# Optimization experiments

Hardware: AMD Instinct MI355X
Metric: run time of the kernel (lower is better)

## Reference

```python
import jax, jax.numpy as jnp
import numpy as np

EPS = 1e-5  # BatchNorm eps (torch default)


def gcn_conv(x, W, b, src, dst, ew, n_nodes):
    """PyG GCNConv with normalize=True, add_self_loops=True (fill_value=1.0).
    Self-loop contribution handled analytically instead of appending edges."""
    xw = x @ W  # [N, out]
    # degree including self-loop weight 1.0 (PyG sums weights at the target node)
    deg = jax.ops.segment_sum(ew, dst, num_segments=n_nodes) + 1.0  # [N]
    dinv = jnp.where(deg > 0, jax.lax.rsqrt(deg), 0.0)
    norm = dinv[src] * ew * dinv[dst]  # [E]
    agg = jax.ops.segment_sum(xw[src] * norm[:, None], dst, num_segments=n_nodes)
    agg = agg + xw * (dinv * dinv)[:, None]  # self-loop message
    return agg + b


def batch_norm(x, gamma, beta):
    m = jnp.mean(x, axis=0)
    v = jnp.var(x, axis=0)  # biased, matches torch BN normalization
    return gamma * (x - m) * jax.lax.rsqrt(v + EPS) + beta


def setup_inputs() -> dict:
    key = jax.random.key(0)
    ks = jax.random.split(key, 12)
    N, E, D_IN, D_H, D_OUT = 100000, 1600000, 128, 128, 40
    x = jax.random.normal(ks[0], (N, D_IN), dtype=jnp.float32)
    edge_index = jax.random.randint(ks[1], (2, E), 0, N, dtype=jnp.int64)
    edge_weight = jax.random.uniform(ks[2], (E,), dtype=jnp.float32)
    def lin(k, fi, fo):
        s = 1.0 / np.sqrt(fi)
        return jax.random.uniform(k, (fi, fo), dtype=jnp.float32, minval=-s, maxval=s)
    return {
        "x": x, "edge_index": edge_index, "edge_weight": edge_weight,
        "W0": lin(ks[3], D_IN, D_H), "b0": jnp.zeros((D_H,), jnp.float32),
        "g0": jnp.ones((D_H,), jnp.float32), "be0": jnp.zeros((D_H,), jnp.float32),
        "W1": lin(ks[4], D_H, D_H), "b1": jnp.zeros((D_H,), jnp.float32),
        "g1": jnp.ones((D_H,), jnp.float32), "be1": jnp.zeros((D_H,), jnp.float32),
        "W2": lin(ks[5], D_H, D_OUT), "b2": jnp.zeros((D_OUT,), jnp.float32),
    }


def reference(x, edge_index, edge_weight, W0, b0, g0, be0, W1, b1, g1, be1, W2, b2):
    n_nodes = x.shape[0]
    src, dst = edge_index[0], edge_index[1]
    # layer 0: GCNConv -> BN -> ReLU (dropout identity: deterministic/eval)
    h = gcn_conv(x, W0, b0, src, dst, edge_weight, n_nodes)
    h = jax.nn.relu(batch_norm(h, g0, be0))
    # layer 1
    h = gcn_conv(h, W1, b1, src, dst, edge_weight, n_nodes)
    h = jax.nn.relu(batch_norm(h, g1, be1))
    # last conv + log_softmax over classes
    h = gcn_conv(h, W2, b2, src, dst, edge_weight, n_nodes)
    return jax.nn.log_softmax(h, axis=-1)
```

## Files before the change

kernel.cpp:

```cpp
#include <hip/hip_runtime.h>
#include <math.h>


#define CHUNK 8192

__device__ __forceinline__ float2 bf2_unpack(unsigned u) {
    float2 r;
    r.x = __uint_as_float(u << 16);
    r.y = __uint_as_float(u & 0xffff0000u);
    return r;
}
__device__ __forceinline__ unsigned bf2_pack(float a, float b) {
    unsigned ua = __float_as_uint(a);
    unsigned ub = __float_as_uint(b);
    ua = (ua + 0x7fffu + ((ua >> 16) & 1u)) >> 16;
    ub = (ub + 0x7fffu + ((ub >> 16) & 1u)) >> 16;
    return ua | (ub << 16);
}

__global__ void k_detect(const unsigned* __restrict__ raw, int nsample, int* __restrict__ flag) {
    int i = blockIdx.x * blockDim.x + threadIdx.x;
    if (i < nsample) {
        if (raw[2 * i + 1] != 0u) atomicOr(flag, 1);
    }
}

__device__ __forceinline__ int edge_src(const unsigned* raw, int e, int E, int is64) {
    return is64 ? (int)raw[2 * (size_t)e] : (int)raw[e];
}
__device__ __forceinline__ int edge_dst(const unsigned* raw, int e, int E, int is64) {
    return is64 ? (int)raw[2 * ((size_t)E + e)] : (int)raw[(size_t)E + e];
}

__global__ __launch_bounds__(256) void k_bhist(const unsigned* __restrict__ raw,
                                               int* __restrict__ bhist, int* __restrict__ chist,
                                               const int* __restrict__ flag,
                                               int E, int NB, int nchunks) {
    __shared__ int h[512];
    int is64 = (*flag == 0);
    for (int c = blockIdx.x; c < nchunks; c += gridDim.x) {
        for (int t = threadIdx.x; t < 512; t += 256) h[t] = 0;
        __syncthreads();
        int base = c * CHUNK;
        int end = (base + CHUNK < E) ? base + CHUNK : E;
        for (int e = base + threadIdx.x; e < end; e += 256) {
            int d = edge_dst(raw, e, E, is64);
            atomicAdd(&h[d >> 8], 1);
        }
        __syncthreads();
        for (int t = threadIdx.x; t < NB; t += 256) {
            int v = h[t];
            chist[(size_t)c * 512 + t] = v;
            if (v) atomicAdd(&bhist[t], v);
        }
        __syncthreads();
    }
}

__global__ __launch_bounds__(512) void k_bscan(const int* __restrict__ bhist,
                                               int* __restrict__ bstart,
                                               int* __restrict__ bcur, int NB) {
    __shared__ int s[512];
    int tid = threadIdx.x;
    int v = (tid < NB) ? bhist[tid] : 0;
    s[tid] = v;
    __syncthreads();
    for (int off = 1; off < 512; off <<= 1) {
        int t = (tid >= off) ? s[tid - off] : 0;
        __syncthreads();
        if (tid >= off) s[tid] += t;
        __syncthreads();
    }
    int ex = s[tid] - v;
    if (tid <= NB) {
        int val = (tid < NB) ? ex : s[NB > 0 ? NB - 1 : 0];
        bstart[tid] = val;
        if (tid < NB) bcur[tid] = val;
    }
}

__global__ __launch_bounds__(256) void k_part(const unsigned* __restrict__ raw,
                                              const float* __restrict__ ew,
                                              const int* __restrict__ chist,
                                              int* __restrict__ bcur, int2* __restrict__ staging,
                                              const int* __restrict__ flag,
                                              int E, int NB, int nchunks) {
    __shared__ int cur[512];
    int is64 = (*flag == 0);
    for (int c = blockIdx.x; c < nchunks; c += gridDim.x) {
        for (int t = threadIdx.x; t < NB; t += 256) {
            int v = chist[(size_t)c * 512 + t];
            cur[t] = v ? atomicAdd(&bcur[t], v) : 0;
        }
        __syncthreads();
        int base = c * CHUNK;
        int end = (base + CHUNK < E) ? base + CHUNK : E;
        for (int e = base + threadIdx.x; e < end; e += 256) {
            int s = edge_src(raw, e, E, is64);
            int d = edge_dst(raw, e, E, is64);
            float w = ew[e];
            int pos = atomicAdd(&cur[d >> 8], 1);
            staging[pos] = make_int2(s | ((d & 255) << 24), __float_as_int(w));
        }
        __syncthreads();
    }
}

__global__ __launch_bounds__(256) void k_bucket(const int* __restrict__ bstart,
                                                const int2* __restrict__ staging,
                                                int* __restrict__ rowptr, float* __restrict__ dinv,
                                                int2* __restrict__ ep, int N, int NB) {
    __shared__ int cnt[256];
    __shared__ float dw[256];
    __shared__ int sc[256];
    __shared__ int cur[256];

    const int b = blockIdx.x;
    const int t = threadIdx.x;
    const int n0 = b << 8;
    const int nn = (N - n0 < 256) ? (N - n0) : 256;
    const int es = bstart[b], ee = bstart[b + 1];

    cnt[t] = 0;
    dw[t] = 0.f;
    __syncthreads();

    for (int j = es + t; j < ee; j += 256) {
        int2 p = staging[j];
        int dl = ((unsigned)p.x) >> 24;
        atomicAdd(&cnt[dl], 1);
        atomicAdd(&dw[dl], __int_as_float(p.y));
    }
    __syncthreads();

    int v = cnt[t];
    sc[t] = v;
    __syncthreads();
    for (int off = 1; off < 256; off <<= 1) {
        int tv = (t >= off) ? sc[t - off] : 0;
        __syncthreads();
        if (t >= off) sc[t] += tv;
        __syncthreads();
    }
    int exoff = sc[t] - v;
    cur[t] = es + exoff;
    if (t < nn) {
        rowptr[n0 + t] = es + exoff;
        dinv[n0 + t] = rsqrtf(dw[t] + 1.0f);
    }
    if (t == 0) rowptr[(n0 + 256 < N) ? (n0 + 256) : N] = ee;
    __syncthreads();

    for (int j = es + t; j < ee; j += 256) {
        int2 p = staging[j];
        int dl = ((unsigned)p.x) >> 24;
        int pos = atomicAdd(&cur[dl], 1);
        ep[pos] = make_int2(p.x & 0x00ffffff, p.y);
    }
}

template <int DOUT, int KC, bool BN>
__global__ __launch_bounds__(256) void k_gemm(
    const float* __restrict__ X, const float* __restrict__ W,
    const float* __restrict__ scale, const float* __restrict__ shift,
    const float* __restrict__ dscale, unsigned* __restrict__ Y, int N)
{
    constexpr int NCH = 128 / KC;
    constexpr int NDW = DOUT / 2;
    __shared__ __align__(16) float Wl[KC * DOUT];
    __shared__ __align__(16) float Xs[4][8 * 128];
    __shared__ float sc_l[128], sh_l[128];

    const int tid = threadIdx.x;
    const int wave = tid >> 6, lane = tid & 63;
    if (BN) {
        if (tid < 128) { sc_l[tid] = scale[tid]; sh_l[tid] = shift[tid]; }
    }
    __syncthreads();

    const int srow = lane >> 3;
    const int skk = (lane & 7) * 16;

    for (int base = blockIdx.x * 32; base < N; base += gridDim.x * 32) {
        {
            int r = base + wave * 8 + srow;
            float4 v[4];
            if (r < N) {
                const float4* p = (const float4*)(X + (size_t)r * 128 + skk);
                v[0] = p[0]; v[1] = p[1]; v[2] = p[2]; v[3] = p[3];
            } else {
                v[0] = v[1] = v[2] = v[3] = make_float4(0.f, 0.f, 0.f, 0.f);
            }
            if (BN) {
                float* vf = (float*)v;
#pragma unroll
                for (int j = 0; j < 16; j++)
                    vf[j] = fmaxf(vf[j] * sc_l[skk + j] + sh_l[skk + j], 0.f);
            }
            float4* q = (float4*)&Xs[wave][srow * 128 + skk];
            q[0] = v[0]; q[1] = v[1]; q[2] = v[2]; q[3] = v[3];
        }

        float acc0[8], acc1[8];
#pragma unroll
        for (int r = 0; r < 8; r++) { acc0[r] = 0.f; acc1[r] = 0.f; }

        for (int ch = 0; ch < NCH; ++ch) {
            __syncthreads();
            for (int idx = tid; idx < KC * DOUT / 4; idx += 256)
                ((float4*)Wl)[idx] = ((const float4*)(W + (size_t)ch * KC * DOUT))[idx];
            __syncthreads();

            for (int k = 0; k < KC; k += 4) {
                float4 a[8];
#pragma unroll
                for (int r = 0; r < 8; r++)
                    a[r] = *(const float4*)&Xs[wave][r * 128 + ch * KC + k];
#pragma unroll
                for (int kk = 0; kk < 4; kk++) {
                    float2 wv = make_float2(0.f, 0.f);
                    if (lane < NDW)
                        wv = *(const float2*)&Wl[(k + kk) * DOUT + 2 * lane];
#pragma unroll
                    for (int r = 0; r < 8; r++) {
                        float av = ((const float*)&a[r])[kk];
                        acc0[r] += av * wv.x;
                        acc1[r] += av * wv.y;
                    }
                }
            }
        }

#pragma unroll
        for (int r = 0; r < 8; r++) {
            int row = base + wave * 8 + r;
            if (row < N && lane < NDW) {
                float rs = dscale[row];
                Y[(size_t)row * NDW + lane] = bf2_pack(acc0[r] * rs, acc1[r] * rs);
            }
        }
    }
}

__global__ __launch_bounds__(256) void k_agg128(
    const unsigned* __restrict__ xw, const int* __restrict__ rowptr,
    const int2* __restrict__ ep, const float* __restrict__ dinv,
    const float* __restrict__ bias, float* __restrict__ h,
    float* __restrict__ bn_sum, float* __restrict__ bn_sq, int N)
{
    __shared__ float redS[512], redQ[512];
    const int lane = threadIdx.x & 63;
    const int wave = threadIdx.x >> 6;
    const int base = blockIdx.x * 64 + wave * 16;
    const float b0 = bias[2 * lane], b1 = bias[2 * lane + 1];
    float s0 = 0.f, s1 = 0.f, q0 = 0.f, q1 = 0.f;

    const int nmax = (N - base < 16) ? (N - base) : 16;
    for (int n = 0; n < nmax; n++) {
        const int i = base + n;
        const int rs = rowptr[i], re = rowptr[i + 1];
        const float di = dinv[i];
        float2 sv = bf2_unpack(xw[(size_t)i * 64 + lane]);
        float acc0 = sv.x, acc1 = sv.y;
        int j = rs;
        for (; j + 4 <= re; j += 4) {
            int2 e0 = ep[j], e1 = ep[j + 1], e2 = ep[j + 2], e3 = ep[j + 3];
            unsigned v0 = xw[(size_t)e0.x * 64 + lane];
            unsigned v1 = xw[(size_t)e1.x * 64 + lane];
            unsigned v2 = xw[(size_t)e2.x * 64 + lane];
            unsigned v3 = xw[(size_t)e3.x * 64 + lane];
            float c0 = __int_as_float(e0.y), c1 = __int_as_float(e1.y);
            float c2 = __int_as_float(e2.y), c3 = __int_as_float(e3.y);
            float2 f0 = bf2_unpack(v0), f1 = bf2_unpack(v1);
            float2 f2 = bf2_unpack(v2), f3 = bf2_unpack(v3);
            acc0 += c0 * f0.x + c1 * f1.x + c2 * f2.x + c3 * f3.x;
            acc1 += c0 * f0.y + c1 * f1.y + c2 * f2.y + c3 * f3.y;
        }
        for (; j < re; j++) {
            int2 e = ep[j];
            float c = __int_as_float(e.y);
            float2 f = bf2_unpack(xw[(size_t)e.x * 64 + lane]);
            acc0 += c * f.x;
            acc1 += c * f.y;
        }
        acc0 = acc0 * di + b0;
        acc1 = acc1 * di + b1;
        *(float2*)&h[(size_t)i * 128 + 2 * lane] = make_float2(acc0, acc1);
        s0 += acc0; s1 += acc1; q0 += acc0 * acc0; q1 += acc1 * acc1;
    }

    redS[wave * 128 + 2 * lane] = s0;
    redS[wave * 128 + 2 * lane + 1] = s1;
    redQ[wave * 128 + 2 * lane] = q0;
    redQ[wave * 128 + 2 * lane + 1] = q1;
    __syncthreads();
    if (threadIdx.x < 128) {
        int f = threadIdx.x;
        float ts = redS[f] + redS[128 + f] + redS[256 + f] + redS[384 + f];
        float tq = redQ[f] + redQ[128 + f] + redQ[256 + f] + redQ[384 + f];
        atomicAdd(&bn_sum[f], ts);
        atomicAdd(&bn_sq[f], tq);
    }
}

__global__ void k_bnfin(const float* __restrict__ bn_sum, const float* __restrict__ bn_sq,
                        const float* __restrict__ gamma, const float* __restrict__ beta,
                        float* __restrict__ scale, float* __restrict__ shift, int N) {
    int f = threadIdx.x;
    float inv = 1.0f / (float)N;
    float m = bn_sum[f] * inv;
    float v = bn_sq[f] * inv - m * m;
    float sc = gamma[f] * rsqrtf(v + 1e-5f);
    scale[f] = sc;
    shift[f] = beta[f] - m * sc;
}

__global__ __launch_bounds__(256) void k_agg40(
    const unsigned* __restrict__ xw, const int* __restrict__ rowptr,
    const int2* __restrict__ ep, const float* __restrict__ dinv,
    const float* __restrict__ bias, float* __restrict__ out, int N)
{
    const int lane = threadIdx.x & 63;
    const int wave = threadIdx.x >> 6;
    const int half = lane >> 5;
    const int col = lane & 31;
    const bool act = col < 20;
    const int base = blockIdx.x * 64 + wave * 16;
    if (base >= N) return;
    const int cc = act ? col : 0;
    const float b0 = act ? bias[2 * col] : 0.f;
    const float b1 = act ? bias[2 * col + 1] : 0.f;

    for (int n = 0; n < 16; n += 2) {
        const int i = base + n + half;
        const bool valid = i < N;
        const int ic = valid ? i : 0;
        const int rs = rowptr[ic];
        int re = rowptr[ic + 1];
        re = valid ? re : rs;
        const float di = dinv[ic];
        float2 sv = bf2_unpack(xw[(size_t)ic * 20 + cc]);
        float acc0 = sv.x, acc1 = sv.y;
        int j = rs;
        for (; j + 4 <= re; j += 4) {
            int2 e0 = ep[j], e1 = ep[j + 1], e2 = ep[j + 2], e3 = ep[j + 3];
            unsigned v0 = xw[(size_t)e0.x * 20 + cc];
            unsigned v1 = xw[(size_t)e1.x * 20 + cc];
            unsigned v2 = xw[(size_t)e2.x * 20 + cc];
            unsigned v3 = xw[(size_t)e3.x * 20 + cc];
            float c0 = __int_as_float(e0.y), c1 = __int_as_float(e1.y);
            float c2 = __int_as_float(e2.y), c3 = __int_as_float(e3.y);
            float2 f0 = bf2_unpack(v0), f1 = bf2_unpack(v1);
            float2 f2 = bf2_unpack(v2), f3 = bf2_unpack(v3);
            acc0 += c0 * f0.x + c1 * f1.x + c2 * f2.x + c3 * f3.x;
            acc1 += c0 * f0.y + c1 * f1.y + c2 * f2.y + c3 * f3.y;
        }
        for (; j < re; j++) {
            int2 e = ep[j];
            float c = __int_as_float(e.y);
            float2 f = bf2_unpack(xw[(size_t)e.x * 20 + cc]);
            acc0 += c * f.x;
            acc1 += c * f.y;
        }
        acc0 = acc0 * di + b0;
        acc1 = acc1 * di + b1;

        float m = act ? fmaxf(acc0, acc1) : -1e30f;
#pragma unroll
        for (int off = 16; off; off >>= 1) m = fmaxf(m, __shfl_xor(m, off));
        float ex = act ? (expf(acc0 - m) + expf(acc1 - m)) : 0.f;
#pragma unroll
        for (int off = 16; off; off >>= 1) ex += __shfl_xor(ex, off);
        float ls = logf(ex);
        if (act && valid)
            *(float2*)&out[(size_t)i * 40 + 2 * col] = make_float2(acc0 - m - ls, acc1 - m - ls);
    }
}

extern "C" void kernel_launch(void* const* d_in, const int* in_sizes, int n_in,
                              void* d_out, int out_size, void* d_ws, size_t ws_size,
                              hipStream_t stream) {
    const float* x   = (const float*)d_in[0];
    const unsigned* ei = (const unsigned*)d_in[1];
    const float* ew  = (const float*)d_in[2];
    const float* W0  = (const float*)d_in[3];
    const float* b0  = (const float*)d_in[4];
    const float* g0  = (const float*)d_in[5];
    const float* be0 = (const float*)d_in[6];
    const float* W1  = (const float*)d_in[7];
    const float* b1  = (const float*)d_in[8];
    const float* g1  = (const float*)d_in[9];
    const float* be1 = (const float*)d_in[10];
    const float* W2  = (const float*)d_in[11];
    const float* b2  = (const float*)d_in[12];

    const int N = in_sizes[0] / 128;
    const int E = in_sizes[2];
    if (N <= 0 || E <= 0) return;
    const int NB = (N + 255) >> 8;
    const int nchunks = (E + CHUNK - 1) / CHUNK;

    char* ws = (char*)d_ws;
    size_t off = 0;
    auto carve = [&](size_t bytes) {
        char* p = ws + off;
        off += (bytes + 511) & ~((size_t)511);
        return p;
    };
    float*    F       = (float*)carve((size_t)N * 128 * 4);
    unsigned* P       = (unsigned*)carve((size_t)N * 64 * 4);
    int2*     ep      = (int2*)carve((size_t)E * 8);
    int2*     staging = (int2*)carve((size_t)E * 8);
    int*      chist   = (int*)carve((size_t)nchunks * 512 * 4);
    int*      rowptr  = (int*)carve((size_t)(N + 1) * 4);
    float*    dinv    = (float*)carve((size_t)N * 4);
    int*      bhist   = (int*)carve(513 * 4);
    int*      bstart  = (int*)carve(513 * 4);
    int*      bcur    = (int*)carve(513 * 4);
    float*    bn      = (float*)carve(512 * 4);
    int*      flag    = (int*)carve(64);

    hipMemsetAsync(bhist, 0, 513 * 4, stream);
    hipMemsetAsync(flag, 0, 4, stream);

    int nsample = E < 4096 ? E : 4096;
    k_detect<<<(nsample + 255) / 256, 256, 0, stream>>>(ei, nsample, flag);
    int pgrid = nchunks < 1024 ? nchunks : 1024;
    k_bhist<<<pgrid, 256, 0, stream>>>(ei, bhist, chist, flag, E, NB, nchunks);
    k_bscan<<<1, 512, 0, stream>>>(bhist, bstart, bcur, NB);
    k_part<<<pgrid, 256, 0, stream>>>(ei, ew, chist, bcur, staging, flag, E, NB, nchunks);
    k_bucket<<<NB, 256, 0, stream>>>(bstart, staging, rowptr, dinv, ep, N, NB);

    const int gemm_grid = 768;
    const int agg_grid = (N + 63) / 64;

    k_gemm<128, 64, false><<<gemm_grid, 256, 0, stream>>>(x, W0, nullptr, nullptr, dinv, P, N);
    hipMemsetAsync(bn, 0, 1024, stream);
    k_agg128<<<agg_grid, 256, 0, stream>>>(P, rowptr, ep, dinv, b0, F, bn, bn + 128, N);
    k_bnfin<<<1, 128, 0, stream>>>(bn, bn + 128, g0, be0, bn + 256, bn + 384, N);

    k_gemm<128, 64, true><<<gemm_grid, 256, 0, stream>>>(F, W1, bn + 256, bn + 384, dinv, P, N);
    hipMemsetAsync(bn, 0, 1024, stream);
    k_agg128<<<agg_grid, 256, 0, stream>>>(P, rowptr, ep, dinv, b1, F, bn, bn + 128, N);
    k_bnfin<<<1, 128, 0, stream>>>(bn, bn + 128, g1, be1, bn + 256, bn + 384, N);

    k_gemm<40, 128, true><<<gemm_grid, 256, 0, stream>>>(F, W2, bn + 256, bn + 384, dinv, P, N);
    k_agg40<<<agg_grid, 256, 0, stream>>>(P, rowptr, ep, dinv, b2, (float*)d_out, N);
}
```

Before: 653.3 us.

## Store hidden activations in bf16, unroll gather by 8 with nontemporal edge loads

The aggregation kernel now writes the post-conv hidden activations as packed bf16 instead of fp32, and the following GEMM reads and unpacks them before applying BN+ReLU. This halves the intermediate write and read traffic between layers. The gather loops in both aggregation kernels are unrolled to 8 edges, and the edge list is read with nontemporal 64-bit loads so more loads are in flight and the cache is less polluted. It adds bf16 rounding of the pre-BN activations, though the BN statistics are still accumulated in fp32 before rounding.

After: 665.5 us. No clear change (+1.9%).

```diff
diff --git a/kernel.cpp b/kernel.cpp
--- a/kernel.cpp
+++ b/kernel.cpp
@@ -161,7 +161,8 @@
 
 template <int DOUT, int KC, bool BN>
 __global__ __launch_bounds__(256) void k_gemm(
-    const float* __restrict__ X, const float* __restrict__ W,
+    const float* __restrict__ X, const unsigned* __restrict__ Xp,
+    const float* __restrict__ W,
     const float* __restrict__ scale, const float* __restrict__ shift,
     const float* __restrict__ dscale, unsigned* __restrict__ Y, int N)
 {
@@ -184,21 +185,38 @@
     for (int base = blockIdx.x * 32; base < N; base += gridDim.x * 32) {
         {
             int r = base + wave * 8 + srow;
-            float4 v[4];
-            if (r < N) {
-                const float4* p = (const float4*)(X + (size_t)r * 128 + skk);
-                v[0] = p[0]; v[1] = p[1]; v[2] = p[2]; v[3] = p[3];
-            } else {
-                v[0] = v[1] = v[2] = v[3] = make_float4(0.f, 0.f, 0.f, 0.f);
-            }
+            float vf[16];
             if (BN) {
-                float* vf = (float*)v;
+                uint4 u0 = make_uint4(0, 0, 0, 0), u1 = u0;
+                if (r < N) {
+                    const uint4* p = (const uint4*)(Xp + (size_t)r * 64 + (lane & 7) * 8);
+                    u0 = p[0]; u1 = p[1];
+                }
+                unsigned uu[8] = {u0.x, u0.y, u0.z, u0.w, u1.x, u1.y, u1.z, u1.w};
+#pragma unroll
+                for (int d = 0; d < 8; d++) {
+                    float2 f = bf2_unpack(uu[d]);
+                    vf[2 * d] = f.x;
+                    vf[2 * d + 1] = f.y;
+                }
 #pragma unroll
                 for (int j = 0; j < 16; j++)
                     vf[j] = fmaxf(vf[j] * sc_l[skk + j] + sh_l[skk + j], 0.f);
+            } else {
+                float4 v[4];
+                if (r < N) {
+                    const float4* p = (const float4*)(X + (size_t)r * 128 + skk);
+                    v[0] = p[0]; v[1] = p[1]; v[2] = p[2]; v[3] = p[3];
+                } else {
+                    v[0] = v[1] = v[2] = v[3] = make_float4(0.f, 0.f, 0.f, 0.f);
+                }
+#pragma unroll
+                for (int j = 0; j < 16; j++) vf[j] = ((const float*)v)[j];
             }
             float4* q = (float4*)&Xs[wave][srow * 128 + skk];
-            q[0] = v[0]; q[1] = v[1]; q[2] = v[2]; q[3] = v[3];
+#pragma unroll
+            for (int d = 0; d < 4; d++)
+                q[d] = make_float4(vf[4 * d], vf[4 * d + 1], vf[4 * d + 2], vf[4 * d + 3]);
         }
 
         float acc0[8], acc1[8];
@@ -244,8 +262,8 @@
 
 __global__ __launch_bounds__(256) void k_agg128(
     const unsigned* __restrict__ xw, const int* __restrict__ rowptr,
-    const int2* __restrict__ ep, const float* __restrict__ dinv,
-    const float* __restrict__ bias, float* __restrict__ h,
+    const unsigned long long* __restrict__ ep, const float* __restrict__ dinv,
+    const float* __restrict__ bias, unsigned* __restrict__ h,
     float* __restrict__ bn_sum, float* __restrict__ bn_sq, int N)
 {
     __shared__ float redS[512], redQ[512];
@@ -263,29 +281,62 @@
         float2 sv = bf2_unpack(xw[(size_t)i * 64 + lane]);
         float acc0 = sv.x, acc1 = sv.y;
         int j = rs;
+        for (; j + 8 <= re; j += 8) {
+            unsigned long long u0 = __builtin_nontemporal_load(ep + j);
+            unsigned long long u1 = __builtin_nontemporal_load(ep + j + 1);
+            unsigned long long u2 = __builtin_nontemporal_load(ep + j + 2);
+            unsigned long long u3 = __builtin_nontemporal_load(ep + j + 3);
+            unsigned long long u4 = __builtin_nontemporal_load(ep + j + 4);
+            unsigned long long u5 = __builtin_nontemporal_load(ep + j + 5);
+            unsigned long long u6 = __builtin_nontemporal_load(ep + j + 6);
+            unsigned long long u7 = __builtin_nontemporal_load(ep + j + 7);
+            unsigned v0 = xw[(size_t)(unsigned)u0 * 64 + lane];
+            unsigned v1 = xw[(size_t)(unsigned)u1 * 64 + lane];
+            unsigned v2 = xw[(size_t)(unsigned)u2 * 64 + lane];
+            unsigned v3 = xw[(size_t)(unsigned)u3 * 64 + lane];
+            unsigned v4 = xw[(size_t)(unsigned)u4 * 64 + lane];
+            unsigned v5 = xw[(size_t)(unsigned)u5 * 64 + lane];
+            unsigned v6 = xw[(size_t)(unsigned)u6 * 64 + lane];
+            unsigned v7 = xw[(size_t)(unsigned)u7 * 64 + lane];
+            float c0 = __int_as_float((int)(u0 >> 32)), c1 = __int_as_float((int)(u1 >> 32));
+            float c2 = __int_as_float((int)(u2 >> 32)), c3 = __int_as_float((int)(u3 >> 32));
+            float c4 = __int_as_float((int)(u4 >> 32)), c5 = __int_as_float((int)(u5 >> 32));
+            float c6 = __int_as_float((int)(u6 >> 32)), c7 = __int_as_float((int)(u7 >> 32));
+            float2 f0 = bf2_unpack(v0), f1 = bf2_unpack(v1);
+            float2 f2 = bf2_unpack(v2), f3 = bf2_unpack(v3);
+            float2 f4 = bf2_unpack(v4), f5 = bf2_unpack(v5);
+            float2 f6 = bf2_unpack(v6), f7 = bf2_unpack(v7);
+            acc0 += c0 * f0.x + c1 * f1.x + c2 * f2.x + c3 * f3.x
+                  + c4 * f4.x + c5 * f5.x + c6 * f6.x + c7 * f7.x;
+            acc1 += c0 * f0.y + c1 * f1.y + c2 * f2.y + c3 * f3.y
+                  + c4 * f4.y + c5 * f5.y + c6 * f6.y + c7 * f7.y;
+        }
         for (; j + 4 <= re; j += 4) {
-            int2 e0 = ep[j], e1 = ep[j + 1], e2 = ep[j + 2], e3 = ep[j + 3];
-            unsigned v0 = xw[(size_t)e0.x * 64 + lane];
-            unsigned v1 = xw[(size_t)e1.x * 64 + lane];
-            unsigned v2 = xw[(size_t)e2.x * 64 + lane];
-            unsigned v3 = xw[(size_t)e3.x * 64 + lane];
-            float c0 = __int_as_float(e0.y), c1 = __int_as_float(e1.y);
-            float c2 = __int_as_float(e2.y), c3 = __int_as_float(e3.y);
+            unsigned long long u0 = __builtin_nontemporal_load(ep + j);
+            unsigned long long u1 = __builtin_nontemporal_load(ep + j + 1);
+            unsigned long long u2 = __builtin_nontemporal_load(ep + j + 2);
+            unsigned long long u3 = __builtin_nontemporal_load(ep + j + 3);
+            unsigned v0 = xw[(size_t)(unsigned)u0 * 64 + lane];
+            unsigned v1 = xw[(size_t)(unsigned)u1 * 64 + lane];
+            unsigned v2 = xw[(size_t)(unsigned)u2 * 64 + lane];
+            unsigned v3 = xw[(size_t)(unsigned)u3 * 64 + lane];
+            float c0 = __int_as_float((int)(u0 >> 32)), c1 = __int_as_float((int)(u1 >> 32));
+            float c2 = __int_as_float((int)(u2 >> 32)), c3 = __int_as_float((int)(u3 >> 32));
             float2 f0 = bf2_unpack(v0), f1 = bf2_unpack(v1);
             float2 f2 = bf2_unpack(v2), f3 = bf2_unpack(v3);
             acc0 += c0 * f0.x + c1 * f1.x + c2 * f2.x + c3 * f3.x;
             acc1 += c0 * f0.y + c1 * f1.y + c2 * f2.y + c3 * f3.y;
         }
         for (; j < re; j++) {
-            int2 e = ep[j];
-            float c = __int_as_float(e.y);
-            float2 f = bf2_unpack(xw[(size_t)e.x * 64 + lane]);
+            unsigned long long u = __builtin_nontemporal_load(ep + j);
+            float c = __int_as_float((int)(u >> 32));
+            float2 f = bf2_unpack(xw[(size_t)(unsigned)u * 64 + lane]);
             acc0 += c * f.x;
             acc1 += c * f.y;
         }
         acc0 = acc0 * di + b0;
         acc1 = acc1 * di + b1;
-        *(float2*)&h[(size_t)i * 128 + 2 * lane] = make_float2(acc0, acc1);
+        __builtin_nontemporal_store(bf2_pack(acc0, acc1), &h[(size_t)i * 64 + lane]);
         s0 += acc0; s1 += acc1; q0 += acc0 * acc0; q1 += acc1 * acc1;
     }
 
@@ -317,7 +368,7 @@
 
 __global__ __launch_bounds__(256) void k_agg40(
     const unsigned* __restrict__ xw, const int* __restrict__ rowptr,
-    const int2* __restrict__ ep, const float* __restrict__ dinv,
+    const unsigned long long* __restrict__ ep, const float* __restrict__ dinv,
     const float* __restrict__ bias, float* __restrict__ out, int N)
 {
     const int lane = threadIdx.x & 63;
@@ -342,23 +393,40 @@
         float2 sv = bf2_unpack(xw[(size_t)ic * 20 + cc]);
         float acc0 = sv.x, acc1 = sv.y;
         int j = rs;
-        for (; j + 4 <= re; j += 4) {
-            int2 e0 = ep[j], e1 = ep[j + 1], e2 = ep[j + 2], e3 = ep[j + 3];
-            unsigned v0 = xw[(size_t)e0.x * 20 + cc];
-            unsigned v1 = xw[(size_t)e1.x * 20 + cc];
-            unsigned v2 = xw[(size_t)e2.x * 20 + cc];
-            unsigned v3 = xw[(size_t)e3.x * 20 + cc];
-            float c0 = __int_as_float(e0.y), c1 = __int_as_float(e1.y);
-            float c2 = __int_as_float(e2.y), c3 = __int_as_float(e3.y);
+        for (; j + 8 <= re; j += 8) {
+            unsigned long long u0 = __builtin_nontemporal_load(ep + j);
+            unsigned long long u1 = __builtin_nontemporal_load(ep + j + 1);
+            unsigned long long u2 = __builtin_nontemporal_load(ep + j + 2);
+            unsigned long long u3 = __builtin_nontemporal_load(ep + j + 3);
+            unsigned long long u4 = __builtin_nontemporal_load(ep + j + 4);
+            unsigned long long u5 = __builtin_nontemporal_load(ep + j + 5);
+            unsigned long long u6 = __builtin_nontemporal_load(ep + j + 6);
+            unsigned long long u7 = __builtin_nontemporal_load(ep + j + 7);
+            unsigned v0 = xw[(size_t)(unsigned)u0 * 20 + cc];
+            unsigned v1 = xw[(size_t)(unsigned)u1 * 20 + cc];
+            unsigned v2 = xw[(size_t)(unsigned)u2 * 20 + cc];
+            unsigned v3 = xw[(size_t)(unsigned)u3 * 20 + cc];
+            unsigned v4 = xw[(size_t)(unsigned)u4 * 20 + cc];
+            unsigned v5 = xw[(size_t)(unsigned)u5 * 20 + cc];
+            unsigned v6 = xw[(size_t)(unsigned)u6 * 20 + cc];
+            unsigned v7 = xw[(size_t)(unsigned)u7 * 20 + cc];
+            float c0 = __int_as_float((int)(u0 >> 32)), c1 = __int_as_float((int)(u1 >> 32));
+            float c2 = __int_as_float((int)(u2 >> 32)), c3 = __int_as_float((int)(u3 >> 32));
+            float c4 = __int_as_float((int)(u4 >> 32)), c5 = __int_as_float((int)(u5 >> 32));
+            float c6 = __int_as_float((int)(u6 >> 32)), c7 = __int_as_float((int)(u7 >> 32));
             float2 f0 = bf2_unpack(v0), f1 = bf2_unpack(v1);
             float2 f2 = bf2_unpack(v2), f3 = bf2_unpack(v3);
-            acc0 += c0 * f0.x + c1 * f1.x + c2 * f2.x + c3 * f3.x;
-            acc1 += c0 * f0.y + c1 * f1.y + c2 * f2.y + c3 * f3.y;
+            float2 f4 = bf2_unpack(v4), f5 = bf2_unpack(v5);
+            float2 f6 = bf2_unpack(v6), f7 = bf2_unpack(v7);
+            acc0 += c0 * f0.x + c1 * f1.x + c2 * f2.x + c3 * f3.x
+                  + c4 * f4.x + c5 * f5.x + c6 * f6.x + c7 * f7.x;
+            acc1 += c0 * f0.y + c1 * f1.y + c2 * f2.y + c3 * f3.y
+                  + c4 * f4.y + c5 * f5.y + c6 * f6.y + c7 * f7.y;
         }
         for (; j < re; j++) {
-            int2 e = ep[j];
-            float c = __int_as_float(e.y);
-            float2 f = bf2_unpack(xw[(size_t)e.x * 20 + cc]);
+            unsigned long long u = __builtin_nontemporal_load(ep + j);
+            float c = __int_as_float((int)(u >> 32));
+            float2 f = bf2_unpack(xw[(size_t)(unsigned)u * 20 + cc]);
             acc0 += c * f.x;
             acc1 += c * f.y;
         }
@@ -407,7 +475,7 @@
         off += (bytes + 511) & ~((size_t)511);
         return p;
     };
-    float*    F       = (float*)carve((size_t)N * 128 * 4);
+    unsigned* F       = (unsigned*)carve((size_t)N * 64 * 4);
     unsigned* P       = (unsigned*)carve((size_t)N * 64 * 4);
     int2*     ep      = (int2*)carve((size_t)E * 8);
     int2*     staging = (int2*)carve((size_t)E * 8);
@@ -433,17 +501,18 @@
 
     const int gemm_grid = 768;
     const int agg_grid = (N + 63) / 64;
-
-    k_gemm<128, 64, false><<<gemm_grid, 256, 0, stream>>>(x, W0, nullptr, nullptr, dinv, P, N);
+    const unsigned long long* epu = (const unsigned long long*)ep;
+
+    k_gemm<128, 64, false><<<gemm_grid, 256, 0, stream>>>(x, nullptr, W0, nullptr, nullptr, dinv, P, N);
     hipMemsetAsync(bn, 0, 1024, stream);
-    k_agg128<<<agg_grid, 256, 0, stream>>>(P, rowptr, ep, dinv, b0, F, bn, bn + 128, N);
+    k_agg128<<<agg_grid, 256, 0, stream>>>(P, rowptr, epu, dinv, b0, F, bn, bn + 128, N);
     k_bnfin<<<1, 128, 0, stream>>>(bn, bn + 128, g0, be0, bn + 256, bn + 384, N);
 
-    k_gemm<128, 64, true><<<gemm_grid, 256, 0, stream>>>(F, W1, bn + 256, bn + 384, dinv, P, N);
+    k_gemm<128, 64, true><<<gemm_grid, 256, 0, stream>>>(nullptr, F, W1, bn + 256, bn + 384, dinv, P, N);
     hipMemsetAsync(bn, 0, 1024, stream);
-    k_agg128<<<agg_grid, 256, 0, stream>>>(P, rowptr, ep, dinv, b1, F, bn, bn + 128, N);
+    k_agg128<<<agg_grid, 256, 0, stream>>>(P, rowptr, epu, dinv, b1, F, bn, bn + 128, N);
     k_bnfin<<<1, 128, 0, stream>>>(bn, bn + 128, g1, be1, bn + 256, bn + 384, N);
 
-    k_gemm<40, 128, true><<<gemm_grid, 256, 0, stream>>>(F, W2, bn + 256, bn + 384, dinv, P, N);
-    k_agg40<<<agg_grid, 256, 0, stream>>>(P, rowptr, ep, dinv, b2, (float*)d_out, N);
-}
+    k_gemm<40, 128, true><<<gemm_grid, 256, 0, stream>>>(nullptr, F, W2, bn + 256, bn + 384, dinv, P, N);
+    k_agg40<<<agg_grid, 256, 0, stream>>>(P, rowptr, epu, dinv, b2, (float*)d_out, N);
+}
```
